# Kernel tuning notes

Measured on AMD Instinct MI355X. Metric: run time of the kernel, lower is better.

The kernel has to match this reference:

```python
import jax, jax.numpy as jnp
import numpy as np

B, L, D, H, SPD = 16, 512, 768, 12, 5
DH = D // H
LN_EPS = 1e-5
CLAMP_MIN = 1e-6


def setup_inputs() -> dict:
    key = jax.random.key(0)
    ks = jax.random.split(key, 8)
    s = 1.0 / np.sqrt(D)
    return {
        "tgt": jax.random.normal(ks[0], (B, L, D), jnp.float32),
        "query_pos": jax.random.normal(ks[1], (B, L, D), jnp.float32),
        "pairwise_locs": jax.random.normal(ks[2], (B, L, L, SPD), jnp.float32),
        "Wq": jax.random.normal(ks[3], (D, D), jnp.float32) * s,
        "bq": jnp.zeros((D,), jnp.float32),
        "Wk": jax.random.normal(ks[4], (D, D), jnp.float32) * s,
        "bk": jnp.zeros((D,), jnp.float32),
        "Wv": jax.random.normal(ks[5], (D, D), jnp.float32) * s,
        "bv": jnp.zeros((D,), jnp.float32),
        "Wo": jax.random.normal(ks[6], (D, D), jnp.float32) * s,
        "bo": jnp.zeros((D,), jnp.float32),
        "Wloc": jax.random.normal(ks[7], (SPD, H), jnp.float32) * (1.0 / np.sqrt(SPD)),
        "bloc": jnp.zeros((H,), jnp.float32),
        "ln_g": jnp.ones((D,), jnp.float32),
        "ln_b": jnp.zeros((D,), jnp.float32),
    }


def _layer_norm(x, g, b):
    mu = jnp.mean(x, axis=-1, keepdims=True)
    var = jnp.mean(jnp.square(x - mu), axis=-1, keepdims=True)
    return g * (x - mu) * jax.lax.rsqrt(var + LN_EPS) + b


def reference(tgt, query_pos, pairwise_locs, Wq, bq, Wk, bk, Wv, bv, Wo, bo, Wloc, bloc, ln_g, ln_b):
    # forward_post path: q = k = tgt + query_pos; v = tgt
    qk_in = tgt + query_pos
    q = (qk_in @ Wq + bq).reshape(B, L, H, DH)   # [B,L,H,DH]
    k = (qk_in @ Wk + bk).reshape(B, L, H, DH)
    v = (tgt @ Wv + bv).reshape(B, L, H, DH)

    scale = np.float32(1.0 / np.sqrt(DH))
    attn = jnp.einsum('blhd,bthd->bhlt', q, k) * scale   # [B,H,L,L]

    # spatial fusion 'mul': relu(Linear(pairwise_locs)) -> log-domain additive bias
    loc_attn = jax.nn.relu(pairwise_locs @ Wloc + bloc)   # [B,L,L,H]
    loc_attn = jnp.transpose(loc_attn, (0, 3, 1, 2))      # [B,H,L,L]
    fused = jax.nn.softmax(jnp.log(jnp.clip(loc_attn, CLAMP_MIN, None)) + attn, axis=-1)

    out = jnp.einsum('bhlt,bthd->blhd', fused, v).reshape(B, L, D)
    out = out @ Wo + bo                                   # attn output (tgt2)

    # residual + (dropout p=0) + LayerNorm
    return _layer_norm(tgt + out, ln_g, ln_b)
```

## Files before the change

kernel.cpp:

```cpp
#include <hip/hip_runtime.h>
#include <math.h>

#define BB 16
#define LL 512
#define DD 768
#define HH 12
#define DHH 64
#define SPDD 5
#define MM (BB*LL)
#define LN_EPS 1e-5f
#define CLAMP_MINV 1e-6f

typedef __attribute__((ext_vector_type(8))) short bf8_t;
typedef __attribute__((ext_vector_type(4))) float f4_t;

__device__ __forceinline__ short f2bf(float x) {
    unsigned u = __builtin_bit_cast(unsigned, x);
    unsigned r = (u + 0x7FFFu + ((u >> 16) & 1u)) >> 16;
    return (short)r;
}
__device__ __forceinline__ float bf2f(short s) {
    unsigned u = ((unsigned)(unsigned short)s) << 16;
    return __builtin_bit_cast(float, u);
}

__device__ __forceinline__ void gld16(const short* g, short* l) {
    __builtin_amdgcn_global_load_lds(
        (const __attribute__((address_space(1))) unsigned int*)g,
        (__attribute__((address_space(3))) unsigned int*)l,
        16, 0, 0);
}

__device__ __forceinline__ float block_sum(float v, float* red, int tid) {
    #pragma unroll
    for (int off = 32; off; off >>= 1) v += __shfl_down(v, off, 64);
    __syncthreads();
    if ((tid & 63) == 0) red[tid >> 6] = v;
    __syncthreads();
    return red[0] + red[1] + red[2] + red[3];
}

__global__ __launch_bounds__(256) void prep_kernel(
    const float* __restrict__ tgt, const float* __restrict__ qpos,
    const float* __restrict__ W0, const float* __restrict__ W1,
    const float* __restrict__ W2, const float* __restrict__ W3,
    short* __restrict__ aqk, short* __restrict__ av,
    short* __restrict__ O0, short* __restrict__ O1,
    short* __restrict__ O2, short* __restrict__ O3)
{
    __shared__ float T[64][65];
    const int t = blockIdx.x;
    if (t < 3072) {
        const size_t base = ((size_t)t * 256 + threadIdx.x) * 8;
        const float4 t0 = *(const float4*)(tgt + base);
        const float4 t1 = *(const float4*)(tgt + base + 4);
        const float4 p0 = *(const float4*)(qpos + base);
        const float4 p1 = *(const float4*)(qpos + base + 4);
        short v[8], q[8];
        v[0] = f2bf(t0.x); v[1] = f2bf(t0.y); v[2] = f2bf(t0.z); v[3] = f2bf(t0.w);
        v[4] = f2bf(t1.x); v[5] = f2bf(t1.y); v[6] = f2bf(t1.z); v[7] = f2bf(t1.w);
        q[0] = f2bf(t0.x + p0.x); q[1] = f2bf(t0.y + p0.y);
        q[2] = f2bf(t0.z + p0.z); q[3] = f2bf(t0.w + p0.w);
        q[4] = f2bf(t1.x + p1.x); q[5] = f2bf(t1.y + p1.y);
        q[6] = f2bf(t1.z + p1.z); q[7] = f2bf(t1.w + p1.w);
        *(bf8_t*)(av + base)  = *(bf8_t*)v;
        *(bf8_t*)(aqk + base) = *(bf8_t*)q;
    } else {
        const int wt = t - 3072;
        const int wi = wt / 144;
        const int rem = wt % 144;
        const float* W; short* O;
        switch (wi) {
            case 0: W = W0; O = O0; break;
            case 1: W = W1; O = O1; break;
            case 2: W = W2; O = O2; break;
            default: W = W3; O = O3; break;
        }
        const int n0 = (rem % 12) * 64, k0 = (rem / 12) * 64;
        const int tid = threadIdx.x;
        {
            const int kk = tid >> 4, nv = (tid & 15) * 4;
            #pragma unroll
            for (int i = 0; i < 4; ++i) {
                const int k = kk + i * 16;
                const float4 v = *(const float4*)(W + (size_t)(k0 + k) * DD + n0 + nv);
                T[k][nv + 0] = v.x; T[k][nv + 1] = v.y;
                T[k][nv + 2] = v.z; T[k][nv + 3] = v.w;
            }
        }
        __syncthreads();
        {
            const int n = tid >> 2, kc = (tid & 3) * 16;
            short tmp[16];
            #pragma unroll
            for (int i = 0; i < 16; ++i) tmp[i] = f2bf(T[kc + i][n]);
            short* dst = O + (size_t)(n0 + n) * DD + k0 + kc;
            *(bf8_t*)dst       = *(bf8_t*)tmp;
            *(bf8_t*)(dst + 8) = *(bf8_t*)(tmp + 8);
        }
    }
}

__global__ __launch_bounds__(256) void gemm_qkv(
    const short* __restrict__ Aqk, const short* __restrict__ Av,
    const short* __restrict__ Wq, const float* __restrict__ bq, short* __restrict__ oq,
    const short* __restrict__ Wk, const float* __restrict__ bk, short* __restrict__ ok,
    const short* __restrict__ Wv, const float* __restrict__ bv, short* __restrict__ ov)
{
    __shared__ short As[128 * 64];
    __shared__ short Bs[128 * 64];
    const int id = blockIdx.y * 18 + blockIdx.x;
    const int xcd = id & 7, j = id >> 3;
    const int by = xcd * 8 + j / 18;
    const int gx = j % 18;
    const int seg = gx / 6;
    const int bx = gx % 6;
    const short* A  = (seg == 2) ? Av : Aqk;
    const short* Wt = (seg == 0) ? Wq : (seg == 1) ? Wk : Wv;
    const float* bias = (seg == 0) ? bq : (seg == 1) ? bk : bv;
    short* out = (seg == 0) ? oq : (seg == 1) ? ok : ov;

    const int n0 = bx * 128, m0 = by * 128;
    const int tid = threadIdx.x;
    const int w = tid >> 6, lane = tid & 63;
    const int quad = lane >> 4, l16 = lane & 15;
    const int wm = w & 1, wn = w >> 1;
    const int sr = w * 8 + (lane >> 3);
    const int sp = lane & 7;

    f4_t acc[4][4];
    #pragma unroll
    for (int i = 0; i < 4; ++i)
        #pragma unroll
        for (int jj = 0; jj < 4; ++jj) acc[i][jj] = (f4_t){0.f, 0.f, 0.f, 0.f};

    for (int k0 = 0; k0 < DD; k0 += 64) {
        __syncthreads();
        #pragma unroll
        for (int ra = 0; ra < 4; ++ra) {
            const int r = sr + ra * 32;
            const int c = sp ^ (r & 7);
            const int ldso = ra * 2048 + w * 512 + lane * 8;
            gld16(A  + (size_t)(m0 + r) * DD + k0 + c * 8, As + ldso);
            gld16(Wt + (size_t)(n0 + r) * DD + k0 + c * 8, Bs + ldso);
        }
        __syncthreads();
        #pragma unroll
        for (int s = 0; s < 2; ++s) {
            bf8_t a[4], b[4];
            #pragma unroll
            for (int i = 0; i < 4; ++i) {
                const int rA = wm * 64 + i * 16 + l16;
                const int pA = (s * 4 + quad) ^ (rA & 7);
                a[i] = *(const bf8_t*)(As + rA * 64 + pA * 8);
                const int rB = wn * 64 + i * 16 + l16;
                const int pB = (s * 4 + quad) ^ (rB & 7);
                b[i] = *(const bf8_t*)(Bs + rB * 64 + pB * 8);
            }
            #pragma unroll
            for (int i = 0; i < 4; ++i)
                #pragma unroll
                for (int jj = 0; jj < 4; ++jj)
                    acc[i][jj] = __builtin_amdgcn_mfma_f32_16x16x32_bf16(a[i], b[jj], acc[i][jj], 0, 0, 0);
        }
    }

    float bvv[4];
    #pragma unroll
    for (int jj = 0; jj < 4; ++jj) bvv[jj] = bias[n0 + wn * 64 + jj * 16 + l16];
    #pragma unroll
    for (int i = 0; i < 4; ++i) {
        #pragma unroll
        for (int jj = 0; jj < 4; ++jj) {
            const int n = n0 + wn * 64 + jj * 16 + l16;
            #pragma unroll
            for (int r = 0; r < 4; ++r) {
                const int m = m0 + wm * 64 + i * 16 + quad * 4 + r;
                const float val = acc[i][jj][r] + bvv[jj];
                const int b_ = m >> 9, l = m & 511;
                const int h = n >> 6, d = n & 63;
                if (seg < 2)
                    out[(((size_t)(b_ * HH + h)) * LL + l) * DHH + d] = f2bf(val);
                else
                    out[(((size_t)(b_ * HH + h)) * DHH + d) * LL + l] = f2bf(val);
            }
        }
    }
}

__global__ __launch_bounds__(256) void gemm_o(
    const short* __restrict__ A, const short* __restrict__ Wt,
    const float* __restrict__ bias, float* __restrict__ out)
{
    __shared__ short As[128 * 64];
    __shared__ short Bs[128 * 64];
    const int id = blockIdx.y * 6 + blockIdx.x;
    const int xcd = id & 7, j = id >> 3;
    const int by = xcd * 8 + j / 6;
    const int bx = j % 6;
    const int n0 = bx * 128, m0 = by * 128;
    const int tid = threadIdx.x;
    const int w = tid >> 6, lane = tid & 63;
    const int quad = lane >> 4, l16 = lane & 15;
    const int wm = w & 1, wn = w >> 1;
    const int sr = w * 8 + (lane >> 3);
    const int sp = lane & 7;

    f4_t acc[4][4];
    #pragma unroll
    for (int i = 0; i < 4; ++i)
        #pragma unroll
        for (int jj = 0; jj < 4; ++jj) acc[i][jj] = (f4_t){0.f, 0.f, 0.f, 0.f};

    for (int k0 = 0; k0 < DD; k0 += 64) {
        __syncthreads();
        #pragma unroll
        for (int ra = 0; ra < 4; ++ra) {
            const int r = sr + ra * 32;
            const int c = sp ^ (r & 7);
            const int ldso = ra * 2048 + w * 512 + lane * 8;
            gld16(A  + (size_t)(m0 + r) * DD + k0 + c * 8, As + ldso);
            gld16(Wt + (size_t)(n0 + r) * DD + k0 + c * 8, Bs + ldso);
        }
        __syncthreads();
        #pragma unroll
        for (int s = 0; s < 2; ++s) {
            bf8_t a[4], b[4];
            #pragma unroll
            for (int i = 0; i < 4; ++i) {
                const int rA = wm * 64 + i * 16 + l16;
                const int pA = (s * 4 + quad) ^ (rA & 7);
                a[i] = *(const bf8_t*)(As + rA * 64 + pA * 8);
                const int rB = wn * 64 + i * 16 + l16;
                const int pB = (s * 4 + quad) ^ (rB & 7);
                b[i] = *(const bf8_t*)(Bs + rB * 64 + pB * 8);
            }
            #pragma unroll
            for (int i = 0; i < 4; ++i)
                #pragma unroll
                for (int jj = 0; jj < 4; ++jj)
                    acc[i][jj] = __builtin_amdgcn_mfma_f32_16x16x32_bf16(a[i], b[jj], acc[i][jj], 0, 0, 0);
        }
    }

    float bvv[4];
    #pragma unroll
    for (int jj = 0; jj < 4; ++jj) bvv[jj] = bias[n0 + wn * 64 + jj * 16 + l16];
    #pragma unroll
    for (int i = 0; i < 4; ++i)
        #pragma unroll
        for (int jj = 0; jj < 4; ++jj) {
            const int n = n0 + wn * 64 + jj * 16 + l16;
            #pragma unroll
            for (int r = 0; r < 4; ++r) {
                const int m = m0 + wm * 64 + i * 16 + quad * 4 + r;
                out[(size_t)m * DD + n] = acc[i][jj][r] + bvv[jj];
            }
        }
}

__global__ __launch_bounds__(256) void attn_mfma(
    const short* __restrict__ Q, const short* __restrict__ K,
    const short* __restrict__ Vt,
    const float* __restrict__ ploc, const float* __restrict__ Wloc,
    const float* __restrict__ bloc, short* __restrict__ out)
{
    __shared__ short Ks[64 * 64];
    __shared__ short Vs[64 * 64];
    __shared__ short bs16[64 * 68];
    __shared__ short Ps[4][16 * 64];

    const int id = blockIdx.x;
    const int xcd = id & 7, slot = id >> 3;
    const int b = xcd + 8 * (slot / 96);
    const int s2 = slot % 96;
    const int h = s2 % 12, qt = s2 / 12;

    const int tid = threadIdx.x;
    const int w = tid >> 6, lane = tid & 63;
    const int quad = lane >> 4, l16 = lane & 15;
    const int q0 = qt * 64;
    const size_t bh = (size_t)b * HH + h;

    float wl[SPDD];
    #pragma unroll
    for (int s = 0; s < SPDD; ++s) wl[s] = Wloc[s * HH + h];
    const float blc = bloc[h];

    const int qr = q0 + w * 16 + l16;
    const bf8_t aq0 = *(const bf8_t*)(Q + (bh * LL + qr) * DHH + quad * 8);
    const bf8_t aq1 = *(const bf8_t*)(Q + (bh * LL + qr) * DHH + quad * 8 + 32);

    f4_t o[4];
    #pragma unroll
    for (int dj = 0; dj < 4; ++dj) o[dj] = (f4_t){0.f, 0.f, 0.f, 0.f};
    float m_row[4], l_row[4];
    #pragma unroll
    for (int r = 0; r < 4; ++r) { m_row[r] = -1e30f; l_row[r] = 0.f; }

    const short* Kg = K  + bh * LL * DHH;
    const short* Vg = Vt + bh * DHH * LL;

    const int srow = tid >> 2;
    const int cb   = (tid & 3) * 2;
    const int sw   = srow & 7;

    for (int t0 = 0; t0 < LL; t0 += 64) {
        __syncthreads();
        {
            const short* src = Kg + (size_t)(t0 + srow) * DHH + cb * 8;
            *(bf8_t*)(Ks + srow * 64 + ((cb ^ sw) * 8))       = *(const bf8_t*)(src);
            *(bf8_t*)(Ks + srow * 64 + (((cb + 1) ^ sw) * 8)) = *(const bf8_t*)(src + 8);
        }
        {
            const short* src = Vg + (size_t)srow * LL + t0 + cb * 8;
            *(bf8_t*)(Vs + srow * 64 + ((cb ^ sw) * 8))       = *(const bf8_t*)(src);
            *(bf8_t*)(Vs + srow * 64 + (((cb + 1) ^ sw) * 8)) = *(const bf8_t*)(src + 8);
        }
        {
            const int l = tid >> 2, ts = (tid & 3) * 16;
            const float* pp = ploc + (((size_t)b * LL + q0 + l) * LL + t0 + ts) * SPDD;
            short o16[16];
            #pragma unroll
            for (int g = 0; g < 4; ++g) {
                float4 c[5];
                const float* src = pp + g * 20;
                #pragma unroll
                for (int i = 0; i < 5; ++i) c[i] = *(const float4*)(src + i * 4);
                const float* pf = (const float*)c;
                #pragma unroll
                for (int e = 0; e < 4; ++e) {
                    float v = blc;
                    #pragma unroll
                    for (int s = 0; s < SPDD; ++s) v += pf[e * SPDD + s] * wl[s];
                    v = fmaxf(fmaxf(v, 0.f), CLAMP_MINV);
                    o16[g * 4 + e] = f2bf(v);
                }
            }
            #pragma unroll
            for (int i = 0; i < 4; ++i)
                *(short4*)(bs16 + l * 68 + ts + i * 4) = *(short4*)(o16 + i * 4);
        }
        __syncthreads();

        f4_t sv[4];
        #pragma unroll
        for (int j = 0; j < 4; ++j) {
            const int rB = j * 16 + l16;
            const int x = rB & 7;
            const bf8_t b0 = *(const bf8_t*)(Ks + rB * 64 + ((quad ^ x) * 8));
            const bf8_t b1 = *(const bf8_t*)(Ks + rB * 64 + (((quad + 4) ^ x) * 8));
            f4_t c = (f4_t){0.f, 0.f, 0.f, 0.f};
            c = __builtin_amdgcn_mfma_f32_16x16x32_bf16(aq0, b0, c, 0, 0, 0);
            c = __builtin_amdgcn_mfma_f32_16x16x32_bf16(aq1, b1, c, 0, 0, 0);
            sv[j] = c;
        }
        #pragma unroll
        for (int j = 0; j < 4; ++j)
            #pragma unroll
            for (int r = 0; r < 4; ++r) sv[j][r] *= 0.125f;

        #pragma unroll
        for (int r = 0; r < 4; ++r) {
            const int lrel = w * 16 + quad * 4 + r;
            float mx = fmaxf(fmaxf(sv[0][r], sv[1][r]), fmaxf(sv[2][r], sv[3][r]));
            mx = fmaxf(mx, __shfl_xor(mx, 1, 16));
            mx = fmaxf(mx, __shfl_xor(mx, 2, 16));
            mx = fmaxf(mx, __shfl_xor(mx, 4, 16));
            mx = fmaxf(mx, __shfl_xor(mx, 8, 16));
            const float mn = fmaxf(m_row[r], mx);
            const float al = __expf(m_row[r] - mn);
            m_row[r] = mn;
            float rs = 0.f;
            #pragma unroll
            for (int j = 0; j < 4; ++j) {
                const float lav = bf2f(bs16[lrel * 68 + j * 16 + l16]);
                const float p = lav * __expf(sv[j][r] - mn);
                sv[j][r] = p;
                rs += p;
            }
            rs += __shfl_xor(rs, 1, 16);
            rs += __shfl_xor(rs, 2, 16);
            rs += __shfl_xor(rs, 4, 16);
            rs += __shfl_xor(rs, 8, 16);
            l_row[r] = l_row[r] * al + rs;
            #pragma unroll
            for (int dj = 0; dj < 4; ++dj) o[dj][r] *= al;
        }
        short* Pw = Ps[w];
        #pragma unroll
        for (int r = 0; r < 4; ++r) {
            const int rp = quad * 4 + r, rp7 = rp & 7;
            #pragma unroll
            for (int j = 0; j < 4; ++j) {
                const int t = j * 16 + l16;
                Pw[rp * 64 + (((t >> 3) ^ rp7) * 8) + (t & 7)] = f2bf(sv[j][r]);
            }
        }
        const int m7 = l16 & 7;
        const bf8_t ap0 = *(const bf8_t*)(Pw + l16 * 64 + ((quad ^ m7) * 8));
        const bf8_t ap1 = *(const bf8_t*)(Pw + l16 * 64 + (((quad + 4) ^ m7) * 8));
        #pragma unroll
        for (int dj = 0; dj < 4; ++dj) {
            const int rB = dj * 16 + l16;
            const int x = rB & 7;
            const bf8_t b0 = *(const bf8_t*)(Vs + rB * 64 + ((quad ^ x) * 8));
            const bf8_t b1 = *(const bf8_t*)(Vs + rB * 64 + (((quad + 4) ^ x) * 8));
            o[dj] = __builtin_amdgcn_mfma_f32_16x16x32_bf16(ap0, b0, o[dj], 0, 0, 0);
            o[dj] = __builtin_amdgcn_mfma_f32_16x16x32_bf16(ap1, b1, o[dj], 0, 0, 0);
        }
    }

    #pragma unroll
    for (int r = 0; r < 4; ++r) {
        const int l = q0 + w * 16 + quad * 4 + r;
        const float inv = 1.f / l_row[r];
        short* op = out + ((size_t)b * LL + l) * DD + h * DHH;
        #pragma unroll
        for (int dj = 0; dj < 4; ++dj)
            op[dj * 16 + l16] = f2bf(o[dj][r] * inv);
    }
}

__global__ __launch_bounds__(256) void ln_kernel(
    const float* __restrict__ x, const float* __restrict__ tgt,
    const float* __restrict__ g, const float* __restrict__ bta,
    float* __restrict__ out)
{
    const int row = blockIdx.x;
    const int tid = threadIdx.x;
    __shared__ float red[4];

    const float* xp = x + (size_t)row * DD;
    const float* tp = tgt + (size_t)row * DD;

    float vals[3];
    float s = 0.f;
    #pragma unroll
    for (int i = 0; i < 3; ++i) {
        const float v = xp[tid + i * 256] + tp[tid + i * 256];
        vals[i] = v;
        s += v;
    }
    s = block_sum(s, red, tid);
    const float mu = s * (1.f / 768.f);

    float vs = 0.f;
    #pragma unroll
    for (int i = 0; i < 3; ++i) {
        const float dv = vals[i] - mu;
        vs += dv * dv;
    }
    vs = block_sum(vs, red, tid);
    const float rstd = rsqrtf(vs * (1.f / 768.f) + LN_EPS);

    #pragma unroll
    for (int i = 0; i < 3; ++i) {
        const int cidx = tid + i * 256;
        out[(size_t)row * DD + cidx] = g[cidx] * (vals[i] - mu) * rstd + bta[cidx];
    }
}

extern "C" void kernel_launch(void* const* d_in, const int* in_sizes, int n_in,
                              void* d_out, int out_size, void* d_ws, size_t ws_size,
                              hipStream_t stream) {
    const float* tgt   = (const float*)d_in[0];
    const float* qpos  = (const float*)d_in[1];
    const float* ploc  = (const float*)d_in[2];
    const float* Wq    = (const float*)d_in[3];
    const float* bq    = (const float*)d_in[4];
    const float* Wk    = (const float*)d_in[5];
    const float* bk    = (const float*)d_in[6];
    const float* Wv    = (const float*)d_in[7];
    const float* bv    = (const float*)d_in[8];
    const float* Wo    = (const float*)d_in[9];
    const float* bo    = (const float*)d_in[10];
    const float* Wloc  = (const float*)d_in[11];
    const float* bloc  = (const float*)d_in[12];
    const float* ln_g  = (const float*)d_in[13];
    const float* ln_b  = (const float*)d_in[14];

    const size_t NQ = (size_t)MM * DD;
    const size_t NW = (size_t)DD * DD;

    short* qb   = (short*)d_ws;
    short* kb   = qb  + NQ;
    short* vtb  = kb  + NQ;
    short* aob  = vtb + NQ;
    short* aqk  = aob + NQ;
    short* av   = aqk + NQ;
    float* pbuf = (float*)aqk;
    short* wqt  = av + NQ;
    short* wkt  = wqt + NW;
    short* wvt  = wkt + NW;
    short* wot  = wvt + NW;

    prep_kernel<<<3648, 256, 0, stream>>>(tgt, qpos, Wq, Wk, Wv, Wo,
                                          aqk, av, wqt, wkt, wvt, wot);

    gemm_qkv<<<dim3(18, 64), 256, 0, stream>>>(aqk, av, wqt, bq, qb,
                                               wkt, bk, kb, wvt, bv, vtb);

    attn_mfma<<<1536, 256, 0, stream>>>(qb, kb, vtb, ploc, Wloc, bloc, aob);

    gemm_o<<<dim3(6, 64), 256, 0, stream>>>(aob, wot, bo, pbuf);

    ln_kernel<<<MM, 256, 0, stream>>>(pbuf, tgt, ln_g, ln_b, (float*)d_out);
}
```

Measured before the change: 392.2 us.

## Prefetch pairwise_locs into registers and load K/V tiles directly to LDS

```diff
diff --git a/kernel.cpp b/kernel.cpp
--- a/kernel.cpp
+++ b/kernel.cpp
@@ -279,6 +279,7 @@
     const int tid = threadIdx.x;
     const int w = tid >> 6, lane = tid & 63;
     const int quad = lane >> 4, l16 = lane & 15;
+    const int l8 = lane >> 3, c8 = lane & 7;
     const int q0 = qt * 64;
     const size_t bh = (size_t)b * HH + h;
 
@@ -301,47 +302,50 @@
     const short* Kg = K  + bh * LL * DHH;
     const short* Vg = Vt + bh * DHH * LL;
 
-    const int srow = tid >> 2;
-    const int cb   = (tid & 3) * 2;
-    const int sw   = srow & 7;
+    const int bl = tid >> 2;
+    const int ts = (tid & 3) * 16;
+    const float* prow = ploc + (size_t)(b * LL + q0 + bl) * LL * SPDD;
+    f4_t pf[20];
+    #define ISSUE_PLOC(TT) do { \
+        const float* _pp = prow + (size_t)((TT) + ts) * SPDD; \
+        _Pragma("unroll") \
+        for (int _i = 0; _i < 20; ++_i) pf[_i] = *(const f4_t*)(_pp + _i * 4); \
+    } while (0)
+    ISSUE_PLOC(0);
 
     for (int t0 = 0; t0 < LL; t0 += 64) {
         __syncthreads();
+        #pragma unroll
+        for (int c = 0; c < 2; ++c) {
+            const int r = w * 16 + c * 8 + l8;
+            const int sc = (c8 ^ (r & 7)) * 8;
+            short* kd = Ks + (w * 16 + c * 8) * 64 + lane * 8;
+            short* vd = Vs + (w * 16 + c * 8) * 64 + lane * 8;
+            gld16(Kg + (size_t)(t0 + r) * DHH + sc, kd);
+            gld16(Vg + (size_t)r * LL + t0 + sc, vd);
+        }
         {
-            const short* src = Kg + (size_t)(t0 + srow) * DHH + cb * 8;
-            *(bf8_t*)(Ks + srow * 64 + ((cb ^ sw) * 8))       = *(const bf8_t*)(src);
-            *(bf8_t*)(Ks + srow * 64 + (((cb + 1) ^ sw) * 8)) = *(const bf8_t*)(src + 8);
-        }
-        {
-            const short* src = Vg + (size_t)srow * LL + t0 + cb * 8;
-            *(bf8_t*)(Vs + srow * 64 + ((cb ^ sw) * 8))       = *(const bf8_t*)(src);
-            *(bf8_t*)(Vs + srow * 64 + (((cb + 1) ^ sw) * 8)) = *(const bf8_t*)(src + 8);
-        }
-        {
-            const int l = tid >> 2, ts = (tid & 3) * 16;
-            const float* pp = ploc + (((size_t)b * LL + q0 + l) * LL + t0 + ts) * SPDD;
             short o16[16];
             #pragma unroll
             for (int g = 0; g < 4; ++g) {
-                float4 c[5];
-                const float* src = pp + g * 20;
-                #pragma unroll
-                for (int i = 0; i < 5; ++i) c[i] = *(const float4*)(src + i * 4);
-                const float* pf = (const float*)c;
                 #pragma unroll
                 for (int e = 0; e < 4; ++e) {
                     float v = blc;
                     #pragma unroll
-                    for (int s = 0; s < SPDD; ++s) v += pf[e * SPDD + s] * wl[s];
+                    for (int s = 0; s < SPDD; ++s) {
+                        const int f = g * 20 + e * SPDD + s;
+                        v += pf[f >> 2][f & 3] * wl[s];
+                    }
                     v = fmaxf(fmaxf(v, 0.f), CLAMP_MINV);
                     o16[g * 4 + e] = f2bf(v);
                 }
             }
             #pragma unroll
             for (int i = 0; i < 4; ++i)
-                *(short4*)(bs16 + l * 68 + ts + i * 4) = *(short4*)(o16 + i * 4);
-        }
-        __syncthreads();
+                *(short4*)(bs16 + bl * 68 + ts + i * 4) = *(short4*)(o16 + i * 4);
+        }
+        __syncthreads();
+        if (t0 + 64 < LL) ISSUE_PLOC(t0 + 64);
 
         f4_t sv[4];
         #pragma unroll
@@ -410,6 +414,7 @@
             o[dj] = __builtin_amdgcn_mfma_f32_16x16x32_bf16(ap1, b1, o[dj], 0, 0, 0);
         }
     }
+    #undef ISSUE_PLOC
 
     #pragma unroll
     for (int r = 0; r < 4; ++r) {
```

Result: no change. 388.8 us (-0.9%).

## Precompute location bias into bf16 buffer inside QKV GEMM launch

Applied to the files above, without the earlier changes.

```diff
diff --git a/kernel.cpp b/kernel.cpp
--- a/kernel.cpp
+++ b/kernel.cpp
@@ -101,15 +101,48 @@
     }
 }
 
-__global__ __launch_bounds__(256) void gemm_qkv(
+__global__ __launch_bounds__(256) void qkv_la(
     const short* __restrict__ Aqk, const short* __restrict__ Av,
     const short* __restrict__ Wq, const float* __restrict__ bq, short* __restrict__ oq,
     const short* __restrict__ Wk, const float* __restrict__ bk, short* __restrict__ ok,
-    const short* __restrict__ Wv, const float* __restrict__ bv, short* __restrict__ ov)
+    const short* __restrict__ Wv, const float* __restrict__ bv, short* __restrict__ ov,
+    const float* __restrict__ ploc, const float* __restrict__ Wloc,
+    const float* __restrict__ bloc, short* __restrict__ la)
 {
     __shared__ short As[128 * 64];
     __shared__ short Bs[128 * 64];
-    const int id = blockIdx.y * 18 + blockIdx.x;
+    const int id = blockIdx.x;
+
+    if (id >= 1152) {
+        const int g   = (id - 1152) * 256 + threadIdx.x;
+        const int tch = g & 63;
+        const int l   = (g >> 6) & 511;
+        const int b   = g >> 15;
+        const int t0  = tch * 8;
+        float p[40];
+        const float* src = ploc + (((size_t)b * LL + l) * LL + t0) * SPDD;
+        #pragma unroll
+        for (int i = 0; i < 10; ++i)
+            *(float4*)(p + i * 4) = *(const float4*)(src + i * 4);
+        #pragma unroll
+        for (int h = 0; h < HH; ++h) {
+            float wl[SPDD];
+            #pragma unroll
+            for (int s = 0; s < SPDD; ++s) wl[s] = Wloc[s * HH + h];
+            const float bl = bloc[h];
+            short o[8];
+            #pragma unroll
+            for (int i = 0; i < 8; ++i) {
+                float v = bl;
+                #pragma unroll
+                for (int s = 0; s < SPDD; ++s) v += p[i * SPDD + s] * wl[s];
+                o[i] = f2bf(fmaxf(v, CLAMP_MINV));
+            }
+            *(bf8_t*)(la + (((size_t)(b * HH + h) * LL + l) * LL + t0)) = *(bf8_t*)o;
+        }
+        return;
+    }
+
     const int xcd = id & 7, j = id >> 3;
     const int by = xcd * 8 + j / 18;
     const int gx = j % 18;
@@ -261,32 +294,22 @@
 
 __global__ __launch_bounds__(256) void attn_mfma(
     const short* __restrict__ Q, const short* __restrict__ K,
-    const short* __restrict__ Vt,
-    const float* __restrict__ ploc, const float* __restrict__ Wloc,
-    const float* __restrict__ bloc, short* __restrict__ out)
+    const short* __restrict__ Vt, const short* __restrict__ LA,
+    short* __restrict__ out)
 {
     __shared__ short Ks[64 * 64];
     __shared__ short Vs[64 * 64];
     __shared__ short bs16[64 * 68];
     __shared__ short Ps[4][16 * 64];
 
-    const int id = blockIdx.x;
-    const int xcd = id & 7, slot = id >> 3;
-    const int b = xcd + 8 * (slot / 96);
-    const int s2 = slot % 96;
-    const int h = s2 % 12, qt = s2 / 12;
-
+    const int h = blockIdx.x % 12, b = blockIdx.x / 12;
+    const int qt = blockIdx.y;
     const int tid = threadIdx.x;
     const int w = tid >> 6, lane = tid & 63;
     const int quad = lane >> 4, l16 = lane & 15;
     const int q0 = qt * 64;
     const size_t bh = (size_t)b * HH + h;
 
-    float wl[SPDD];
-    #pragma unroll
-    for (int s = 0; s < SPDD; ++s) wl[s] = Wloc[s * HH + h];
-    const float blc = bloc[h];
-
     const int qr = q0 + w * 16 + l16;
     const bf8_t aq0 = *(const bf8_t*)(Q + (bh * LL + qr) * DHH + quad * 8);
     const bf8_t aq1 = *(const bf8_t*)(Q + (bh * LL + qr) * DHH + quad * 8 + 32);
@@ -300,6 +323,7 @@
 
     const short* Kg = K  + bh * LL * DHH;
     const short* Vg = Vt + bh * DHH * LL;
+    const short* Bg = LA + (bh * LL + q0) * LL;
 
     const int srow = tid >> 2;
     const int cb   = (tid & 3) * 2;
@@ -319,27 +343,10 @@
         }
         {
             const int l = tid >> 2, ts = (tid & 3) * 16;
-            const float* pp = ploc + (((size_t)b * LL + q0 + l) * LL + t0 + ts) * SPDD;
-            short o16[16];
-            #pragma unroll
-            for (int g = 0; g < 4; ++g) {
-                float4 c[5];
-                const float* src = pp + g * 20;
-                #pragma unroll
-                for (int i = 0; i < 5; ++i) c[i] = *(const float4*)(src + i * 4);
-                const float* pf = (const float*)c;
-                #pragma unroll
-                for (int e = 0; e < 4; ++e) {
-                    float v = blc;
-                    #pragma unroll
-                    for (int s = 0; s < SPDD; ++s) v += pf[e * SPDD + s] * wl[s];
-                    v = fmaxf(fmaxf(v, 0.f), CLAMP_MINV);
-                    o16[g * 4 + e] = f2bf(v);
-                }
-            }
+            const short* src = Bg + (size_t)l * LL + t0 + ts;
             #pragma unroll
             for (int i = 0; i < 4; ++i)
-                *(short4*)(bs16 + l * 68 + ts + i * 4) = *(short4*)(o16 + i * 4);
+                *(short4*)(bs16 + l * 68 + ts + i * 4) = *(const short4*)(src + i * 4);
         }
         __syncthreads();
 
@@ -355,10 +362,6 @@
             c = __builtin_amdgcn_mfma_f32_16x16x32_bf16(aq1, b1, c, 0, 0, 0);
             sv[j] = c;
         }
-        #pragma unroll
-        for (int j = 0; j < 4; ++j)
-            #pragma unroll
-            for (int r = 0; r < 4; ++r) sv[j][r] *= 0.125f;
 
         #pragma unroll
         for (int r = 0; r < 4; ++r) {
@@ -368,14 +371,14 @@
             mx = fmaxf(mx, __shfl_xor(mx, 2, 16));
             mx = fmaxf(mx, __shfl_xor(mx, 4, 16));
             mx = fmaxf(mx, __shfl_xor(mx, 8, 16));
-            const float mn = fmaxf(m_row[r], mx);
+            const float mn = fmaxf(m_row[r], mx * 0.125f);
             const float al = __expf(m_row[r] - mn);
             m_row[r] = mn;
             float rs = 0.f;
             #pragma unroll
             for (int j = 0; j < 4; ++j) {
                 const float lav = bf2f(bs16[lrel * 68 + j * 16 + l16]);
-                const float p = lav * __expf(sv[j][r] - mn);
+                const float p = lav * __expf(__builtin_fmaf(sv[j][r], 0.125f, -mn));
                 sv[j][r] = p;
                 rs += p;
             }
@@ -494,14 +497,16 @@
     short* wkt  = wqt + NW;
     short* wvt  = wkt + NW;
     short* wot  = wvt + NW;
+    short* lab  = wot + NW;
 
     prep_kernel<<<3648, 256, 0, stream>>>(tgt, qpos, Wq, Wk, Wv, Wo,
                                           aqk, av, wqt, wkt, wvt, wot);
 
-    gemm_qkv<<<dim3(18, 64), 256, 0, stream>>>(aqk, av, wqt, bq, qb,
-                                               wkt, bk, kb, wvt, bv, vtb);
-
-    attn_mfma<<<1536, 256, 0, stream>>>(qb, kb, vtb, ploc, Wloc, bloc, aob);
+    qkv_la<<<3200, 256, 0, stream>>>(aqk, av, wqt, bq, qb,
+                                     wkt, bk, kb, wvt, bv, vtb,
+                                     ploc, Wloc, bloc, lab);
+
+    attn_mfma<<<dim3(192, 8), 256, 0, stream>>>(qb, kb, vtb, lab, aob);
 
     gemm_o<<<dim3(6, 64), 256, 0, stream>>>(aob, wot, bo, pbuf);
 
```

Result: faster. 346.6 us (-11.6%).
